# Kernel optimization log

Measured on AMD Instinct MI355X. Metric: run time of the kernel, lower is better.

Reference implementation:

```python
import jax, jax.numpy as jnp
import numpy as np

T, H, E, K = 16384, 2880, 128, 4

def setup_inputs() -> dict:
    key = jax.random.key(0)
    k1, k2, k3 = jax.random.split(key, 3)
    return {
        "hidden_states": jax.random.normal(k1, (T, H), dtype=jnp.float32),
        "weight": jax.random.normal(k2, (E, H), dtype=jnp.float32) * 0.02,
        "bias": jax.random.normal(k3, (E,), dtype=jnp.float32) * 0.02,
    }

def reference(hidden_states, weight, bias):
    x = hidden_states.reshape(-1, weight.shape[1])            # [T, H]
    logits = jnp.einsum('th,eh->te', x, weight) + bias        # [T, E]
    top_val, top_idx = jax.lax.top_k(logits, K)               # sorted desc, [T, K]
    top_val = jax.nn.softmax(top_val, axis=-1)
    rows = jnp.arange(logits.shape[0])[:, None]
    scores = jnp.zeros_like(logits).at[rows, top_idx].set(top_val)
    return scores, top_idx
```

## Files before the change

kernel.cpp:

```cpp
#include <hip/hip_runtime.h>
#include <math.h>


#define T_TOK 16384
#define HDIM  2880
#define EEXP  128
#define KTOP  4

#define TM   16
#define NT   256
#define KC   64
#define NCH  (HDIM / KC)
#define XBUF 2048
#define TAU  4e-3f

typedef __attribute__((ext_vector_type(8))) _Float16 f16x8;
typedef __attribute__((ext_vector_type(4))) float    f32x4;

#define MFMA(a, b, c) __builtin_amdgcn_mfma_f32_16x16x32_f16((a), (b), (c), 0, 0, 0)

__global__ __launch_bounds__(256) void w_cvt(
    const float* __restrict__ w, char* __restrict__ wp)
{
    const int gid  = blockIdx.x * 256 + threadIdx.x;
    const int lane = gid & 63;
    const int q    = gid >> 6;
    const int ks   = q & 1;
    const int q2   = q >> 1;
    const int c    = q2 % NCH;
    const int F    = q2 / NCH;
    const int e    = F * 16 + (lane & 15);
    const int k0   = c * 64 + ks * 32 + (lane >> 4) * 8;

    const float* src = w + (size_t)e * HDIM + k0;
    float4 v0 = *(const float4*)(src);
    float4 v1 = *(const float4*)(src + 4);
    union { _Float16 h[8]; uint4 u; } H;
    H.h[0] = (_Float16)v0.x; H.h[1] = (_Float16)v0.y;
    H.h[2] = (_Float16)v0.z; H.h[3] = (_Float16)v0.w;
    H.h[4] = (_Float16)v1.x; H.h[5] = (_Float16)v1.y;
    H.h[6] = (_Float16)v1.z; H.h[7] = (_Float16)v1.w;
    const int tile = (F * NCH + c) * 2 + ks;
    *(uint4*)(wp + (size_t)tile * 1024 + lane * 16) = H.u;
}

static __device__ __forceinline__ void cvt_write128(char* base, int off, float4 v) {
    union { _Float16 h[4]; uint2 u; } U;
    U.h[0] = (_Float16)v.x; U.h[1] = (_Float16)v.y;
    U.h[2] = (_Float16)v.z; U.h[3] = (_Float16)v.w;
    *(uint2*)(base + off) = U.u;
}

__global__ __launch_bounds__(NT, 4) void router_fused(
    const float* __restrict__ x, const char* __restrict__ wp,
    const float* __restrict__ w, const float* __restrict__ bias,
    float* __restrict__ out)
{
    __shared__ char smem[10240];
    const int tid  = threadIdx.x;
    const int tok0 = blockIdx.x * TM;
    const int lane = tid & 63;
    const int wv   = tid >> 6;
    const int r    = lane & 15;
    const int g    = lane >> 4;

    char* xb0 = smem;
    char* xb1 = smem + XBUF;
    char* xb2 = smem + 2 * XBUF;

    int xoff;
    const float* xptr;
    {
        int row = tid >> 4, c4 = tid & 15;
        xoff = row * 128 + ((((c4 >> 1) ^ (row & 7)) << 4) | ((c4 & 1) << 3));
        xptr = x + (size_t)(tok0 + row) * HDIM + c4 * 4;
    }

    int aoff[2];
    {
        int row = r;
#pragma unroll
        for (int ks = 0; ks < 2; ++ks)
            aoff[ks] = row * 128 + (((ks * 4 + g) ^ (row & 7)) << 4);
    }

    f32x4 a00 = {0.f, 0.f, 0.f, 0.f}, a01 = a00;

#define LOADX(pf, cc) do { pf = *(const float4*)(xptr + (cc) * KC); } while (0)
#define WRITEX(pf, bb) do { cvt_write128((bb), xoff, pf); } while (0)

#define LOADW(W, cc) do {                                             \
        _Pragma("unroll")                                             \
        for (int F2 = 0; F2 < 2; ++F2)                                \
        _Pragma("unroll")                                             \
        for (int ks_ = 0; ks_ < 2; ++ks_)                             \
            W[F2*2 + ks_] = *(const f16x8*)(wp +                      \
                (size_t)(((wv*2 + F2) * NCH + (cc)) * 2 + ks_) * 1024 \
                + lane * 16); } while (0)

#define MFMA_CHUNK(cb, W) do {                                        \
        _Pragma("unroll")                                             \
        for (int ks_ = 0; ks_ < 2; ++ks_) {                           \
            f16x8 a0 = *(const f16x8*)((cb) + aoff[ks_]);             \
            a00 = MFMA(a0, W[ks_],     a00);                          \
            a01 = MFMA(a0, W[2 + ks_], a01);                          \
        } } while (0)

    float4 pfA, pfB, pfC;
    f16x8 wA[4], wB[4], wC[4];

    LOADX(pfA, 0); LOADX(pfB, 1); LOADX(pfC, 2);
    LOADW(wA, 0); LOADW(wB, 1);
    WRITEX(pfA, xb0);
    __syncthreads();

    for (int c = 0; c < NCH; c += 3) {
        if (c + 3 < NCH) LOADX(pfA, c + 3);
        LOADW(wC, c + 2);
        MFMA_CHUNK(xb0, wA);
        WRITEX(pfB, xb1);
        __syncthreads();
        if (c + 3 < NCH) LOADW(wA, c + 3);
        if (c + 4 < NCH) LOADX(pfB, c + 4);
        MFMA_CHUNK(xb1, wB);
        WRITEX(pfC, xb2);
        __syncthreads();
        if (c + 4 < NCH) LOADW(wB, c + 4);
        if (c + 5 < NCH) LOADX(pfC, c + 5);
        MFMA_CHUNK(xb2, wC);
        if (c + 3 < NCH) WRITEX(pfA, xb0);
        __syncthreads();
    }

    float* logitsL = (float*)smem;
    {
        const float bv0 = bias[wv * 32 + r];
        const float bv1 = bias[wv * 32 + 16 + r];
#pragma unroll
        for (int q = 0; q < 4; ++q) {
            int tok = g * 4 + q;
            int e0 = wv * 32 + r, e1 = e0 + 16;
            logitsL[tok * 130 + e0] = a00[q] + bv0;
            logitsL[tok * 130 + e1] = a01[q] + bv1;
        }
    }
    float*  cvf = (float*) (smem + 8320);
    int*    cie = (int*)   (smem + 8832);
    int*    flg = (int*)   (smem + 9344);
    double* svd = (double*)(smem + 9408);
    int*    sid = (int*)   (smem + 9920);
    double* cvd = (double*)(smem + 10176);
    __syncthreads();

    if (tid < 128) {
        const int t = tid >> 3, s = tid & 7;
        float v[8]; int id[8];
#pragma unroll
        for (int k = 0; k < 8; ++k) { v[k] = -3.4e38f; id[k] = 0x7fffffff; }
        for (int jj = 0; jj < 16; ++jj) {
            float lv = logitsL[t * 130 + s * 16 + jj];
            int   e  = s * 16 + jj;
            bool gt[8];
#pragma unroll
            for (int k = 0; k < 8; ++k)
                gt[k] = (lv > v[k]) || (lv == v[k] && e < id[k]);
#pragma unroll
            for (int k = 7; k >= 1; --k)
                if (gt[k - 1]) { v[k] = v[k - 1]; id[k] = id[k - 1]; }
#pragma unroll
            for (int k = 0; k < 8; ++k) {
                bool put = gt[k] && (k == 0 || !gt[k - 1]);
                if (put) { v[k] = lv; id[k] = e; }
            }
        }
#pragma unroll
        for (int rd = 0; rd < 8; ++rd) {
            float hv = v[0]; int hi = id[0];
#pragma unroll
            for (int off = 1; off < 8; off <<= 1) {
                float ov = __shfl_xor(hv, off);
                int   oi = __shfl_xor(hi, off);
                if (ov > hv || (ov == hv && oi < hi)) { hv = ov; hi = oi; }
            }
            if (s == 0) { cvf[t * 8 + rd] = hv; cie[t * 8 + rd] = hi; }
            bool mine = (v[0] == hv) && (id[0] == hi);
            if (mine) {
#pragma unroll
                for (int k = 0; k < 7; ++k) { v[k] = v[k + 1]; id[k] = id[k + 1]; }
                v[7] = -3.4e38f; id[7] = 0x7fffffff;
            }
        }
    }
    __syncthreads();

    if (tid < TM) {
        float gmin = 3.4e38f;
#pragma unroll
        for (int k = 0; k < 4; ++k)
            gmin = fminf(gmin, cvf[tid * 8 + k] - cvf[tid * 8 + k + 1]);
        flg[tid] = (gmin < TAU);
    }
    if (tid < 64) {
        int t2 = tid >> 2, k = tid & 3;
        svd[t2 * 4 + k] = (double)cvf[t2 * 8 + k];
        sid[t2 * 4 + k] = cie[t2 * 8 + k];
    }
    __syncthreads();

    for (int ts = 0; ts < TM; ++ts) {
        if (!flg[ts]) continue;
#pragma unroll
        for (int h2 = 0; h2 < 2; ++h2) {
            const int cand = wv * 2 + h2;
            const int ce = cie[ts * 8 + cand];
            const float4* xr = (const float4*)(x + (size_t)(tok0 + ts) * HDIM);
            const float4* wr = (const float4*)(w + (size_t)ce * HDIM);
            double q0 = 0.0, q1 = 0.0, q2 = 0.0, q3 = 0.0;
            for (int i2 = 0; i2 < 12; ++i2) {
                int fi = lane + i2 * 64;
                if (fi < HDIM / 4) {
                    float4 xv = xr[fi];
                    float4 wv4 = wr[fi];
                    q0 = fma((double)xv.x, (double)wv4.x, q0);
                    q1 = fma((double)xv.y, (double)wv4.y, q1);
                    q2 = fma((double)xv.z, (double)wv4.z, q2);
                    q3 = fma((double)xv.w, (double)wv4.w, q3);
                }
            }
            double accd = (q0 + q2) + (q1 + q3);
#pragma unroll
            for (int off = 32; off > 0; off >>= 1)
                accd += __shfl_xor(accd, off);
            if (lane == 0) cvd[cand] = accd + (double)bias[ce];
        }
        __syncthreads();
        if (tid < 8) {
            double mv = cvd[tid]; int mi2 = cie[ts * 8 + tid];
            int rk = 0;
#pragma unroll
            for (int j2 = 0; j2 < 8; ++j2) {
                double oj = cvd[j2];
                rk += (oj > mv) || (oj == mv && cie[ts * 8 + j2] < mi2);
            }
            if (rk < 4) { svd[ts * 4 + rk] = mv; sid[ts * 4 + rk] = mi2; }
        }
        __syncthreads();
    }

    float* srow = (float*)smem;
    float4 z4 = make_float4(0.f, 0.f, 0.f, 0.f);
#pragma unroll
    for (int i = 0; i < 2; ++i)
        ((float4*)srow)[tid + i * NT] = z4;
    __syncthreads();

    if (tid < TM) {
        double m  = svd[tid * 4];
        double e0 = exp(svd[tid * 4 + 0] - m), e1 = exp(svd[tid * 4 + 1] - m);
        double e2 = exp(svd[tid * 4 + 2] - m), e3 = exp(svd[tid * 4 + 3] - m);
        double inv = 1.0 / ((e0 + e1) + (e2 + e3));
        float* oidx = out + (size_t)T_TOK * EEXP + (size_t)(tok0 + tid) * KTOP;
        int i0 = sid[tid * 4 + 0], i1 = sid[tid * 4 + 1];
        int i2 = sid[tid * 4 + 2], i3 = sid[tid * 4 + 3];
        oidx[0] = (float)i0; oidx[1] = (float)i1;
        oidx[2] = (float)i2; oidx[3] = (float)i3;
        srow[tid * EEXP + i0] = (float)(e0 * inv);
        srow[tid * EEXP + i1] = (float)(e1 * inv);
        srow[tid * EEXP + i2] = (float)(e2 * inv);
        srow[tid * EEXP + i3] = (float)(e3 * inv);
    }
    __syncthreads();

    float4* orow = (float4*)(out + (size_t)tok0 * EEXP);
#pragma unroll
    for (int i = 0; i < 2; ++i)
        orow[tid + i * NT] = ((float4*)srow)[tid + i * NT];
}

extern "C" void kernel_launch(void* const* d_in, const int* in_sizes, int n_in,
                              void* d_out, int out_size, void* d_ws, size_t ws_size,
                              hipStream_t stream) {
    const float* x    = (const float*)d_in[0];
    const float* w    = (const float*)d_in[1];
    const float* bias = (const float*)d_in[2];
    float* out        = (float*)d_out;
    char*  wp         = (char*)d_ws;

    hipLaunchKernelGGL(w_cvt, dim3(180), dim3(256), 0, stream, w, wp);
    hipLaunchKernelGGL(router_fused, dim3(T_TOK / TM), dim3(NT), 0, stream,
                       x, wp, w, bias, out);
}
```

Before: 84.28 us.

## Stage full token rows in LDS and split experts across eight waves

The kernel no longer runs a triple-buffered chunked pipeline over K. Each block now loads all 16 token rows (full hidden dim, converted to fp16) into about 92KB of LDS up front. It then runs 8 waves, each computing one 16-expert tile over the whole K range with direct global weight loads. The aim is to drop the per-chunk barriers and gain more waves per block, but the large LDS footprint limits occupancy to about one block per CU. Global loads also no longer overlap with MFMA work inside a block.

```diff
diff --git a/kernel.cpp b/kernel.cpp
--- a/kernel.cpp
+++ b/kernel.cpp
@@ -7,12 +7,11 @@
 #define EEXP  128
 #define KTOP  4
 
-#define TM   16
-#define NT   256
-#define KC   64
-#define NCH  (HDIM / KC)
-#define XBUF 2048
-#define TAU  4e-3f
+#define TM    16
+#define NT    512
+#define NCH   45
+#define LDROW 5776
+#define TAU   4e-3f
 
 typedef __attribute__((ext_vector_type(8))) _Float16 f16x8;
 typedef __attribute__((ext_vector_type(4))) float    f32x4;
@@ -44,19 +43,12 @@
     *(uint4*)(wp + (size_t)tile * 1024 + lane * 16) = H.u;
 }
 
-static __device__ __forceinline__ void cvt_write128(char* base, int off, float4 v) {
-    union { _Float16 h[4]; uint2 u; } U;
-    U.h[0] = (_Float16)v.x; U.h[1] = (_Float16)v.y;
-    U.h[2] = (_Float16)v.z; U.h[3] = (_Float16)v.w;
-    *(uint2*)(base + off) = U.u;
-}
-
-__global__ __launch_bounds__(NT, 4) void router_fused(
+__global__ __launch_bounds__(NT, 1) void router_fused(
     const float* __restrict__ x, const char* __restrict__ wp,
     const float* __restrict__ w, const float* __restrict__ bias,
     float* __restrict__ out)
 {
-    __shared__ char smem[10240];
+    __shared__ char smem[TM * LDROW];
     const int tid  = threadIdx.x;
     const int tok0 = blockIdx.x * TM;
     const int lane = tid & 63;
@@ -64,84 +56,44 @@
     const int r    = lane & 15;
     const int g    = lane >> 4;
 
-    char* xb0 = smem;
-    char* xb1 = smem + XBUF;
-    char* xb2 = smem + 2 * XBUF;
-
-    int xoff;
-    const float* xptr;
+    for (int f = tid; f < TM * 720; f += NT) {
+        int row = f / 720, fq = f % 720;
+        float4 v = *(const float4*)(x + (size_t)(tok0 + row) * HDIM + fq * 4);
+        union { _Float16 h[4]; uint2 u; } U;
+        U.h[0] = (_Float16)v.x; U.h[1] = (_Float16)v.y;
+        U.h[2] = (_Float16)v.z; U.h[3] = (_Float16)v.w;
+        int slot = fq >> 1;
+        int phys = slot ^ (row & 7);
+        *(uint2*)(smem + row * LDROW + phys * 16 + (fq & 1) * 8) = U.u;
+    }
+    __syncthreads();
+
+    f32x4 acc = {0.f, 0.f, 0.f, 0.f};
     {
-        int row = tid >> 4, c4 = tid & 15;
-        xoff = row * 128 + ((((c4 >> 1) ^ (row & 7)) << 4) | ((c4 & 1) << 3));
-        xptr = x + (size_t)(tok0 + row) * HDIM + c4 * 4;
-    }
-
-    int aoff[2];
-    {
-        int row = r;
-#pragma unroll
-        for (int ks = 0; ks < 2; ++ks)
-            aoff[ks] = row * 128 + (((ks * 4 + g) ^ (row & 7)) << 4);
-    }
-
-    f32x4 a00 = {0.f, 0.f, 0.f, 0.f}, a01 = a00;
-
-#define LOADX(pf, cc) do { pf = *(const float4*)(xptr + (cc) * KC); } while (0)
-#define WRITEX(pf, bb) do { cvt_write128((bb), xoff, pf); } while (0)
-
-#define LOADW(W, cc) do {                                             \
-        _Pragma("unroll")                                             \
-        for (int F2 = 0; F2 < 2; ++F2)                                \
-        _Pragma("unroll")                                             \
-        for (int ks_ = 0; ks_ < 2; ++ks_)                             \
-            W[F2*2 + ks_] = *(const f16x8*)(wp +                      \
-                (size_t)(((wv*2 + F2) * NCH + (cc)) * 2 + ks_) * 1024 \
-                + lane * 16); } while (0)
-
-#define MFMA_CHUNK(cb, W) do {                                        \
-        _Pragma("unroll")                                             \
-        for (int ks_ = 0; ks_ < 2; ++ks_) {                           \
-            f16x8 a0 = *(const f16x8*)((cb) + aoff[ks_]);             \
-            a00 = MFMA(a0, W[ks_],     a00);                          \
-            a01 = MFMA(a0, W[2 + ks_], a01);                          \
-        } } while (0)
-
-    float4 pfA, pfB, pfC;
-    f16x8 wA[4], wB[4], wC[4];
-
-    LOADX(pfA, 0); LOADX(pfB, 1); LOADX(pfC, 2);
-    LOADW(wA, 0); LOADW(wB, 1);
-    WRITEX(pfA, xb0);
-    __syncthreads();
-
-    for (int c = 0; c < NCH; c += 3) {
-        if (c + 3 < NCH) LOADX(pfA, c + 3);
-        LOADW(wC, c + 2);
-        MFMA_CHUNK(xb0, wA);
-        WRITEX(pfB, xb1);
-        __syncthreads();
-        if (c + 3 < NCH) LOADW(wA, c + 3);
-        if (c + 4 < NCH) LOADX(pfB, c + 4);
-        MFMA_CHUNK(xb1, wB);
-        WRITEX(pfC, xb2);
-        __syncthreads();
-        if (c + 4 < NCH) LOADW(wB, c + 4);
-        if (c + 5 < NCH) LOADX(pfC, c + 5);
-        MFMA_CHUNK(xb2, wC);
-        if (c + 3 < NCH) WRITEX(pfA, xb0);
-        __syncthreads();
-    }
+        const int  arow  = r * LDROW;
+        const int  rp    = r & 7;
+        const char* wbase = wp + lane * 16 + (size_t)(wv * NCH) * 2048;
+#pragma unroll 5
+        for (int c = 0; c < NCH; ++c) {
+#pragma unroll
+            for (int ks = 0; ks < 2; ++ks) {
+                int slot = c * 8 + ks * 4 + g;
+                f16x8 a = *(const f16x8*)(smem + arow + ((slot ^ rp) << 4));
+                f16x8 W = *(const f16x8*)(wbase + (size_t)(c * 2 + ks) * 1024);
+                acc = MFMA(a, W, acc);
+            }
+        }
+    }
+    __syncthreads();
 
     float* logitsL = (float*)smem;
     {
-        const float bv0 = bias[wv * 32 + r];
-        const float bv1 = bias[wv * 32 + 16 + r];
+        const int e  = wv * 16 + r;
+        const float bv = bias[e];
 #pragma unroll
         for (int q = 0; q < 4; ++q) {
             int tok = g * 4 + q;
-            int e0 = wv * 32 + r, e1 = e0 + 16;
-            logitsL[tok * 130 + e0] = a00[q] + bv0;
-            logitsL[tok * 130 + e1] = a01[q] + bv1;
+            logitsL[tok * 130 + e] = acc[q] + bv;
         }
     }
     float*  cvf = (float*) (smem + 8320);
@@ -209,10 +161,8 @@
 
     for (int ts = 0; ts < TM; ++ts) {
         if (!flg[ts]) continue;
-#pragma unroll
-        for (int h2 = 0; h2 < 2; ++h2) {
-            const int cand = wv * 2 + h2;
-            const int ce = cie[ts * 8 + cand];
+        {
+            const int ce = cie[ts * 8 + wv];
             const float4* xr = (const float4*)(x + (size_t)(tok0 + ts) * HDIM);
             const float4* wr = (const float4*)(w + (size_t)ce * HDIM);
             double q0 = 0.0, q1 = 0.0, q2 = 0.0, q3 = 0.0;
@@ -231,7 +181,7 @@
 #pragma unroll
             for (int off = 32; off > 0; off >>= 1)
                 accd += __shfl_xor(accd, off);
-            if (lane == 0) cvd[cand] = accd + (double)bias[ce];
+            if (lane == 0) cvd[wv] = accd + (double)bias[ce];
         }
         __syncthreads();
         if (tid < 8) {
@@ -248,10 +198,10 @@
     }
 
     float* srow = (float*)smem;
-    float4 z4 = make_float4(0.f, 0.f, 0.f, 0.f);
-#pragma unroll
-    for (int i = 0; i < 2; ++i)
-        ((float4*)srow)[tid + i * NT] = z4;
+    if (tid < 512) {
+        if (tid < TM * EEXP / 4)
+            ((float4*)srow)[tid] = make_float4(0.f, 0.f, 0.f, 0.f);
+    }
     __syncthreads();
 
     if (tid < TM) {
@@ -272,9 +222,7 @@
     __syncthreads();
 
     float4* orow = (float4*)(out + (size_t)tok0 * EEXP);
-#pragma unroll
-    for (int i = 0; i < 2; ++i)
-        orow[tid + i * NT] = ((float4*)srow)[tid + i * NT];
+    orow[tid] = ((float4*)srow)[tid];
 }
 
 extern "C" void kernel_launch(void* const* d_in, const int* in_sizes, int n_in,
```

New measurement: 146.1 us. 73.4% more time.
